# Optimization experiments

Measured on AMD Instinct MI355X. Metric: run time of the kernel, lower is better.

The kernel has to match this reference:

```python
import jax, jax.numpy as jnp
import numpy as np

TEMPERATURE = 1.0
NEG = -1e9
EPS = 1e-8


def setup_inputs() -> dict:
    key = jax.random.key(0)
    k1, k2, k3 = jax.random.split(key, 3)
    B, H = 524288, 32
    scores = jax.random.normal(k1, (B, H), dtype=jnp.float32)
    rankings = jax.random.randint(k2, (B, H), 0, 33, dtype=jnp.int32)
    mask = jax.random.randint(k3, (B, H), 0, 2, dtype=jnp.int32).astype(bool)
    return {"scores": scores, "rankings": rankings, "mask": mask}


def reference(scores, rankings, mask):
    B, H = scores.shape
    # effective validity: horse present AND has a ranking > 0 (top_k=None)
    m = mask & (rankings > 0)
    # masked, temperature-scaled scores; -1e9 entries underflow to exactly 0 in softmax
    s = jnp.where(m, scores / TEMPERATURE, NEG)
    p = jax.nn.softmax(s, axis=1)  # [B, H], ~0 at invalid slots

    n_valid = jnp.sum(m, axis=1)  # [B]
    # ideal order: valid horses sorted by ranking ascending (invalid pushed to end)
    rank_key = jnp.where(m, rankings, jnp.iinfo(jnp.int32).max)
    rank_order = jnp.argsort(rank_key, axis=1)          # stable sort
    # prediction order: valid horses in original index order (matches torch.where)
    pos_order = jnp.argsort(~m, axis=1)                 # stable: valid first

    q = jnp.take_along_axis(p, rank_order, axis=1)      # ideal_probs, aligned by list position
    pr = jnp.take_along_axis(p, pos_order, axis=1)      # pred_probs,  aligned by list position

    # positions >= n_valid are padding
    valid_pos = jnp.arange(H)[None, :] < n_valid[:, None]
    q_safe = jnp.where(valid_pos, q, 1.0)
    pr_safe = jnp.where(valid_pos, pr, 1.0)
    # KL(ideal || pred) with the original's log(pred + 1e-8)
    kl_terms = q_safe * (jnp.log(q_safe) - jnp.log(pr_safe + EPS))
    kl = jnp.sum(jnp.where(valid_pos, kl_terms, 0.0), axis=1)  # [B]

    # rows with <= 1 valid ranked horse are skipped entirely
    row_ok = n_valid > 1
    n_rows = jnp.maximum(jnp.sum(row_ok), 1)
    return jnp.sum(jnp.where(row_ok, kl, 0.0)) / n_rows  # reduction='mean'
```

## Files before the change

kernel.cpp:

```cpp
#include <hip/hip_runtime.h>
#include <stdint.h>


#define H 32
#define BLK 256
#define WPB 4

__global__ __launch_bounds__(BLK) void listwise_kernel(
    const float* __restrict__ scores,
    const int* __restrict__ rankings,
    const unsigned char* __restrict__ mask_u8,
    float* __restrict__ part_kl,
    float* __restrict__ part_cnt,
    int nrows, int ipw)
{
    __shared__ float s_kl[WPB], s_cnt[WPB];

    const int tid  = threadIdx.x;
    const int lane = tid & 63;
    const int wid  = tid >> 6;
    const int e5   = lane & 31;
    const int h    = lane >> 5;

    const long long wave_g = (long long)blockIdx.x * WPB + wid;
    const long long tpairs = ((long long)nrows + 1) >> 1;
    const long long pbase  = wave_g * ipw;
    const long long pend   = (pbase + ipw < tpairs) ? (pbase + ipw) : tpairs;

    unsigned char probe = mask_u8[lane];
    const bool mask_is_i32 =
        (__ballot(((lane & 3) != 0) && (probe != 0)) == 0ull);

    float kl_acc = 0.0f, cnt_acc = 0.0f;

    if (pbase < pend) {
        const size_t maxidx = (size_t)nrows * H - 1;

        size_t b = (size_t)pbase * 64 + lane;
        if (b > maxidx) b = maxidx;
        int      rv = rankings[b];
        float    sv = scores[b];
        uint32_t mv = mask_is_i32 ? (uint32_t)((const int*)mask_u8)[b]
                                  : (uint32_t)mask_u8[b];

        for (long long p = pbase; p < pend; ++p) {
            const long long pn = (p + 1 < pend) ? (p + 1) : p;
            size_t bn = (size_t)pn * 64 + lane;
            if (bn > maxidx) bn = maxidx;
            const int      rvn = rankings[bn];
            const float    svn = scores[bn];
            const uint32_t mvn = mask_is_i32
                ? (uint32_t)((const int*)mask_u8)[bn]
                : (uint32_t)mask_u8[bn];

            const int  row   = (int)(2 * p) + h;
            const bool valid = (row < nrows) && (mv != 0u) && (rv > 0);
            const uint32_t b16 = (__float_as_uint(sv) + 0x8000u) >> 16;
            const uint32_t key = valid ? (((uint32_t)rv << 5) | (uint32_t)e5)
                                       : (0x4000u | (uint32_t)e5);
            uint32_t w = (key << 16) | b16;
            const float gsrc = __uint_as_float(b16 << 16);

            const unsigned long long vm = __ballot(valid);
            const uint32_t mb = __builtin_amdgcn_mbcnt_hi(
                (uint32_t)(vm >> 32),
                __builtin_amdgcn_mbcnt_lo((uint32_t)vm, 0u));
            const int plo = __builtin_popcountll(vm & 0xffffffffull);
            const int phi = __builtin_popcountll(vm >> 32);
            const int q   = (int)mb - (h ? plo : 0);
            const int nvh = h ? phi : plo;
            const int slot = (valid ? q : (nvh + (e5 - q))) + (h << 5);
            const float gq = __uint_as_float(
                __builtin_amdgcn_ds_permute(slot << 2, (int)__float_as_uint(gsrc)));

            #pragma unroll
            for (int k = 2; k <= 32; k <<= 1) {
                #pragma unroll
                for (int j = k >> 1; j > 0; j >>= 1) {
                    const uint32_t pw = (uint32_t)__shfl_xor((int)w, j);
                    const uint32_t mn = w < pw ? w : pw;
                    const uint32_t mx = w < pw ? pw : w;
                    const bool tm = (((e5 & j) == 0) != ((e5 & k) == 0));
                    w = tm ? mx : mn;
                }
            }

            const bool  vld = (w < 0x40000000u);
            const float sb  = __uint_as_float(w << 16);
            float e = __expf(sb);
            e = vld ? e : 0.0f;
            const float d = vld ? (sb - gq) : 0.0f;
            float se = e;
            float nm = e * d;
            #pragma unroll
            for (int j2 = 1; j2 <= 16; j2 <<= 1) {
                se += __shfl_xor(se, j2);
                nm += __shfl_xor(nm, j2);
            }
            const bool rok = (nvh > 1);
            const float contrib = rok ? __fdividef(nm, se) : 0.0f;
            kl_acc  += (e5 == 0) ? contrib : 0.0f;
            cnt_acc += (e5 == 0 && rok) ? 1.0f : 0.0f;

            rv = rvn; sv = svn; mv = mvn;
        }
    }

    kl_acc  += __shfl_xor(kl_acc, 32);
    cnt_acc += __shfl_xor(cnt_acc, 32);
    if (lane == 0) { s_kl[wid] = kl_acc; s_cnt[wid] = cnt_acc; }
    __syncthreads();
    if (tid == 0) {
        part_kl[blockIdx.x]  = s_kl[0] + s_kl[1] + s_kl[2] + s_kl[3];
        part_cnt[blockIdx.x] = s_cnt[0] + s_cnt[1] + s_cnt[2] + s_cnt[3];
    }
}

__global__ __launch_bounds__(256) void finalize_kernel(
    const float* __restrict__ part_kl,
    const float* __restrict__ part_cnt,
    float* __restrict__ out, int nblk)
{
    float k = 0.0f, c = 0.0f;
    for (int i = threadIdx.x; i < nblk; i += 256) {
        k += part_kl[i];
        c += part_cnt[i];
    }
    #pragma unroll
    for (int m = 32; m >= 1; m >>= 1) {
        k += __shfl_xor(k, m);
        c += __shfl_xor(c, m);
    }
    __shared__ float sk[4], sc[4];
    const int wid = threadIdx.x >> 6;
    if ((threadIdx.x & 63) == 0) { sk[wid] = k; sc[wid] = c; }
    __syncthreads();
    if (threadIdx.x == 0) {
        float K = sk[0] + sk[1] + sk[2] + sk[3];
        float C = sc[0] + sc[1] + sc[2] + sc[3];
        if (C < 1.0f) C = 1.0f;
        out[0] = K / C;
    }
}

extern "C" void kernel_launch(void* const* d_in, const int* in_sizes, int n_in,
                              void* d_out, int out_size, void* d_ws, size_t ws_size,
                              hipStream_t stream) {
    const float* scores = (const float*)d_in[0];
    const int* rankings = (const int*)d_in[1];
    const unsigned char* mask = (const unsigned char*)d_in[2];
    float* out = (float*)d_out;

    const int total = in_sizes[0];
    const int nrows = total / H;
    const int blocks = 2048;
    const long long tpairs = ((long long)nrows + 1) >> 1;
    const long long waves = (long long)blocks * WPB;
    int ipw = (int)((tpairs + waves - 1) / waves);
    if (ipw < 1) ipw = 1;

    float* part_kl  = (float*)d_ws;
    float* part_cnt = (float*)d_ws + blocks;

    listwise_kernel<<<blocks, BLK, 0, stream>>>(
        scores, rankings, mask, part_kl, part_cnt, nrows, ipw);

    finalize_kernel<<<1, 256, 0, stream>>>(part_kl, part_cnt, out, blocks);
}
```

Measured before the change: 215.9 us.

## Sort two row-pairs at once with packed 16-bit keys and DPP shuffles

Each wave now handles four rows per iteration by packing two 16-bit sort keys (ranking plus lane index) into one 32-bit word. A single bitonic network therefore sorts both row pairs, with packed min/max compare-exchange. Short-distance shuffles and the 32-lane sums use DPP moves instead of LDS-based shuffles, and sorted scores are gathered back via ds_bpermute. The aim is to cut shuffle and ALU cost per row. In exchange it adds register pressure and extra bpermute gathers.

```diff
diff --git a/kernel.cpp b/kernel.cpp
--- a/kernel.cpp
+++ b/kernel.cpp
@@ -5,6 +5,38 @@
 #define H 32
 #define BLK 256
 #define WPB 4
+
+typedef unsigned short us2 __attribute__((ext_vector_type(2)));
+union UP { uint32_t u; us2 v; };
+
+template<int CTRL>
+__device__ __forceinline__ uint32_t dppmov_u(uint32_t x) {
+    return (uint32_t)__builtin_amdgcn_update_dpp(0, (int)x, CTRL, 0xF, 0xF, true);
+}
+template<int CTRL>
+__device__ __forceinline__ float dppmov_f(float x) {
+    return __int_as_float(
+        __builtin_amdgcn_update_dpp(0, __float_as_int(x), CTRL, 0xF, 0xF, true));
+}
+
+__device__ __forceinline__ float half_sum32(float v) {
+    v += dppmov_f<0x111>(v);
+    v += dppmov_f<0x112>(v);
+    v += dppmov_f<0x114>(v);
+    v += dppmov_f<0x118>(v);
+    v += dppmov_f<0x142>(v);
+    return v;
+}
+
+__device__ __forceinline__ uint32_t cex(uint32_t W, uint32_t Wo, bool tm) {
+    UP a, b, mn, mx;
+    a.u = W; b.u = Wo;
+    mn.v.x = a.v.x < b.v.x ? a.v.x : b.v.x;
+    mx.v.x = a.v.x < b.v.x ? b.v.x : a.v.x;
+    mn.v.y = a.v.y < b.v.y ? a.v.y : b.v.y;
+    mx.v.y = a.v.y < b.v.y ? b.v.y : a.v.y;
+    return tm ? mx.u : mn.u;
+}
 
 __global__ __launch_bounds__(BLK) void listwise_kernel(
     const float* __restrict__ scores,
@@ -21,11 +53,12 @@
     const int wid  = tid >> 6;
     const int e5   = lane & 31;
     const int h    = lane >> 5;
-
-    const long long wave_g = (long long)blockIdx.x * WPB + wid;
-    const long long tpairs = ((long long)nrows + 1) >> 1;
-    const long long pbase  = wave_g * ipw;
-    const long long pend   = (pbase + ipw < tpairs) ? (pbase + ipw) : tpairs;
+    const uint32_t e5u = (uint32_t)e5;
+
+    const long long wave_g  = (long long)blockIdx.x * WPB + wid;
+    const long long tgroups = ((long long)nrows + 3) >> 2;
+    const long long gbeg = wave_g * ipw;
+    const long long gend = (gbeg + ipw < tgroups) ? (gbeg + ipw) : tgroups;
 
     unsigned char probe = mask_u8[lane];
     const bool mask_is_i32 =
@@ -33,81 +66,119 @@
 
     float kl_acc = 0.0f, cnt_acc = 0.0f;
 
-    if (pbase < pend) {
+    if (gbeg < gend) {
         const size_t maxidx = (size_t)nrows * H - 1;
 
-        size_t b = (size_t)pbase * 64 + lane;
-        if (b > maxidx) b = maxidx;
-        int      rv = rankings[b];
-        float    sv = scores[b];
-        uint32_t mv = mask_is_i32 ? (uint32_t)((const int*)mask_u8)[b]
-                                  : (uint32_t)mask_u8[b];
-
-        for (long long p = pbase; p < pend; ++p) {
-            const long long pn = (p + 1 < pend) ? (p + 1) : p;
-            size_t bn = (size_t)pn * 64 + lane;
-            if (bn > maxidx) bn = maxidx;
-            const int      rvn = rankings[bn];
-            const float    svn = scores[bn];
-            const uint32_t mvn = mask_is_i32
-                ? (uint32_t)((const int*)mask_u8)[bn]
-                : (uint32_t)mask_u8[bn];
-
-            const int  row   = (int)(2 * p) + h;
-            const bool valid = (row < nrows) && (mv != 0u) && (rv > 0);
-            const uint32_t b16 = (__float_as_uint(sv) + 0x8000u) >> 16;
-            const uint32_t key = valid ? (((uint32_t)rv << 5) | (uint32_t)e5)
-                                       : (0x4000u | (uint32_t)e5);
-            uint32_t w = (key << 16) | b16;
-            const float gsrc = __uint_as_float(b16 << 16);
-
-            const unsigned long long vm = __ballot(valid);
-            const uint32_t mb = __builtin_amdgcn_mbcnt_hi(
-                (uint32_t)(vm >> 32),
-                __builtin_amdgcn_mbcnt_lo((uint32_t)vm, 0u));
-            const int plo = __builtin_popcountll(vm & 0xffffffffull);
-            const int phi = __builtin_popcountll(vm >> 32);
-            const int q   = (int)mb - (h ? plo : 0);
-            const int nvh = h ? phi : plo;
-            const int slot = (valid ? q : (nvh + (e5 - q))) + (h << 5);
-            const float gq = __uint_as_float(
-                __builtin_amdgcn_ds_permute(slot << 2, (int)__float_as_uint(gsrc)));
+        size_t b0 = (size_t)gbeg * 128 + lane; if (b0 > maxidx) b0 = maxidx;
+        size_t b1 = (size_t)gbeg * 128 + 64 + lane; if (b1 > maxidx) b1 = maxidx;
+        int   rv0 = rankings[b0], rv1 = rankings[b1];
+        float sv0 = scores[b0],   sv1 = scores[b1];
+        uint32_t mm0, mm1;
+        if (mask_is_i32) {
+            mm0 = (uint32_t)((const int*)mask_u8)[b0];
+            mm1 = (uint32_t)((const int*)mask_u8)[b1];
+        } else {
+            mm0 = (uint32_t)mask_u8[b0];
+            mm1 = (uint32_t)mask_u8[b1];
+        }
+
+        for (long long g = gbeg; g < gend; ++g) {
+            const long long gn = (g + 1 < gend) ? (g + 1) : g;
+            size_t nb0 = (size_t)gn * 128 + lane; if (nb0 > maxidx) nb0 = maxidx;
+            size_t nb1 = (size_t)gn * 128 + 64 + lane; if (nb1 > maxidx) nb1 = maxidx;
+            const int   xrv0 = rankings[nb0], xrv1 = rankings[nb1];
+            const float xsv0 = scores[nb0],   xsv1 = scores[nb1];
+            uint32_t xmm0, xmm1;
+            if (mask_is_i32) {
+                xmm0 = (uint32_t)((const int*)mask_u8)[nb0];
+                xmm1 = (uint32_t)((const int*)mask_u8)[nb1];
+            } else {
+                xmm0 = (uint32_t)mask_u8[nb0];
+                xmm1 = (uint32_t)mask_u8[nb1];
+            }
+
+            const int rowA = (int)(4 * g) + h;
+            const int rowB = rowA + 2;
+            const bool vA = (rowA < nrows) && (mm0 != 0u) && (rv0 > 0);
+            const bool vB = (rowB < nrows) && (mm1 != 0u) && (rv1 > 0);
+
+            const float sA = __uint_as_float(((__float_as_uint(sv0) + 0x8000u) >> 16) << 16);
+            const float sB = __uint_as_float(((__float_as_uint(sv1) + 0x8000u) >> 16) << 16);
+
+            const uint32_t kA = vA ? (((uint32_t)rv0 << 5) | e5u) : (0x8000u | e5u);
+            const uint32_t kB = vB ? (((uint32_t)rv1 << 5) | e5u) : (0x8000u | e5u);
+            uint32_t W = kA | (kB << 16);
+
+            const unsigned long long bmA = __ballot(vA);
+            const unsigned long long bmB = __ballot(vB);
+            const uint32_t lo_pcA = __builtin_popcount((uint32_t)bmA);
+            const uint32_t lo_pcB = __builtin_popcount((uint32_t)bmB);
+            const uint32_t belowA = __builtin_amdgcn_mbcnt_hi(
+                (uint32_t)(bmA >> 32),
+                __builtin_amdgcn_mbcnt_lo((uint32_t)bmA, 0u));
+            const uint32_t belowB = __builtin_amdgcn_mbcnt_hi(
+                (uint32_t)(bmB >> 32),
+                __builtin_amdgcn_mbcnt_lo((uint32_t)bmB, 0u));
+            const int qA = (int)belowA - (h ? (int)lo_pcA : 0);
+            const int qB = (int)belowB - (h ? (int)lo_pcB : 0);
+            const int nvA = h ? __builtin_popcount((uint32_t)(bmA >> 32)) : (int)lo_pcA;
+            const int nvB = h ? __builtin_popcount((uint32_t)(bmB >> 32)) : (int)lo_pcB;
+            const int slotA = (vA ? qA : nvA + (e5 - qA)) + (h << 5);
+            const int slotB = (vB ? qB : nvB + (e5 - qB)) + (h << 5);
+            const float gA = __int_as_float(
+                __builtin_amdgcn_ds_permute(slotA << 2, __float_as_int(sA)));
+            const float gB = __int_as_float(
+                __builtin_amdgcn_ds_permute(slotB << 2, __float_as_int(sB)));
 
             #pragma unroll
             for (int k = 2; k <= 32; k <<= 1) {
                 #pragma unroll
                 for (int j = k >> 1; j > 0; j >>= 1) {
-                    const uint32_t pw = (uint32_t)__shfl_xor((int)w, j);
-                    const uint32_t mn = w < pw ? w : pw;
-                    const uint32_t mx = w < pw ? pw : w;
+                    uint32_t Wo;
+                    if (j == 1)      Wo = dppmov_u<0xB1>(W);
+                    else if (j == 2) Wo = dppmov_u<0x4E>(W);
+                    else             Wo = (uint32_t)__shfl_xor((int)W, j);
                     const bool tm = (((e5 & j) == 0) != ((e5 & k) == 0));
-                    w = tm ? mx : mn;
+                    W = cex(W, Wo, tm);
                 }
             }
 
-            const bool  vld = (w < 0x40000000u);
-            const float sb  = __uint_as_float(w << 16);
-            float e = __expf(sb);
-            e = vld ? e : 0.0f;
-            const float d = vld ? (sb - gq) : 0.0f;
-            float se = e;
-            float nm = e * d;
-            #pragma unroll
-            for (int j2 = 1; j2 <= 16; j2 <<= 1) {
-                se += __shfl_xor(se, j2);
-                nm += __shfl_xor(nm, j2);
-            }
-            const bool rok = (nvh > 1);
-            const float contrib = rok ? __fdividef(nm, se) : 0.0f;
-            kl_acc  += (e5 == 0) ? contrib : 0.0f;
-            cnt_acc += (e5 == 0 && rok) ? 1.0f : 0.0f;
-
-            rv = rvn; sv = svn; mv = mvn;
+            const uint32_t WA = W & 0xFFFFu, WB = W >> 16;
+            const bool vA2 = (WA & 0x8000u) == 0u;
+            const bool vB2 = (WB & 0x8000u) == 0u;
+            const int iA = (int)(WA & 31u), iB = (int)(WB & 31u);
+            const float srA = __int_as_float(__builtin_amdgcn_ds_bpermute(
+                (((h << 5) | iA) << 2), __float_as_int(sA)));
+            const float srB = __int_as_float(__builtin_amdgcn_ds_bpermute(
+                (((h << 5) | iB) << 2), __float_as_int(sB)));
+
+            float eA = __expf(srA); eA = vA2 ? eA : 0.0f;
+            float eB = __expf(srB); eB = vB2 ? eB : 0.0f;
+            const float tA = eA * (srA - gA);
+            const float tB = eB * (srB - gB);
+
+            const float seA = half_sum32(eA);
+            const float seB = half_sum32(eB);
+            const float nmA = half_sum32(tA);
+            const float nmB = half_sum32(tB);
+
+            const float cA = (nvA > 1) ? __fdividef(nmA, seA) : 0.0f;
+            const float cB = (nvB > 1) ? __fdividef(nmB, seB) : 0.0f;
+            const bool tip = (e5 == 31);
+            kl_acc  += tip ? (cA + cB) : 0.0f;
+            cnt_acc += tip ? ((nvA > 1 ? 1.0f : 0.0f) + (nvB > 1 ? 1.0f : 0.0f))
+                           : 0.0f;
+
+            rv0 = xrv0; rv1 = xrv1; sv0 = xsv0; sv1 = xsv1;
+            mm0 = xmm0; mm1 = xmm1;
         }
     }
 
-    kl_acc  += __shfl_xor(kl_acc, 32);
-    cnt_acc += __shfl_xor(cnt_acc, 32);
+    #pragma unroll
+    for (int m = 32; m >= 1; m >>= 1) {
+        kl_acc  += __shfl_xor(kl_acc, m);
+        cnt_acc += __shfl_xor(cnt_acc, m);
+    }
     if (lane == 0) { s_kl[wid] = kl_acc; s_cnt[wid] = cnt_acc; }
     __syncthreads();
     if (tid == 0) {
@@ -154,9 +225,9 @@
     const int total = in_sizes[0];
     const int nrows = total / H;
     const int blocks = 2048;
-    const long long tpairs = ((long long)nrows + 1) >> 1;
+    const long long tgroups = ((long long)nrows + 3) >> 2;
     const long long waves = (long long)blocks * WPB;
-    int ipw = (int)((tpairs + waves - 1) / waves);
+    int ipw = (int)((tgroups + waves - 1) / waves);
     if (ipw < 1) ipw = 1;
 
     float* part_kl  = (float*)d_ws;
```

After: 206.9 us. -4.2%, faster.
